# Kernel tuning notes

Measured on AMD Instinct MI355X. Metric: run time of the kernel, lower is better.

## Reference

```python
import jax, jax.numpy as jnp
import numpy as np

B, T, C = 2, 2048, 1024
E = 8            # num_experts
K = 2            # num_active (top-k)
H = 4 * C        # expert hidden dim


def setup_inputs() -> dict:
    key = jax.random.key(0)
    ks = jax.random.split(key, 8)
    s = 0.02
    return {
        "x": jax.random.normal(ks[0], (B, T, C), dtype=jnp.float32),
        "Wg": jax.random.normal(ks[1], (C, E), dtype=jnp.float32) * s,
        "bg": jnp.zeros((E,), dtype=jnp.float32),
        "W1": jax.random.normal(ks[2], (E, C, H), dtype=jnp.float32) * s,
        "b1": jnp.zeros((E, H), dtype=jnp.float32),
        "W2": jax.random.normal(ks[3], (E, H, C), dtype=jnp.float32) * s,
        "b2": jnp.zeros((E, C), dtype=jnp.float32),
    }


def reference(x, Wg, bg, W1, b1, W2, b2):
    Bs, Ts, Cs = x.shape
    x_flat = x.reshape(-1, Cs)                       # [N, C]
    gate_logits = x_flat @ Wg + bg                   # [N, E]
    gates = jax.nn.softmax(gate_logits, axis=-1)
    w, idx = jax.lax.top_k(gates, K)                 # [N, K]
    w = w / jnp.sum(w, axis=-1, keepdims=True)
    # combine[n, e] = sum_k w[n,k] * (idx[n,k] == e); zero for unrouted experts,
    # so weighting the dense per-expert output reproduces the masked scatter-add.
    combine = jnp.sum(jax.nn.one_hot(idx, E, dtype=x.dtype) * w[..., None], axis=1)  # [N, E]
    out = jnp.zeros_like(x_flat)
    for e in range(E):  # small fixed expert loop; GEMM-dominated
        h = jax.nn.gelu(x_flat @ W1[e] + b1[e], approximate=False)  # [N, H]
        y = h @ W2[e] + b2[e]                                       # [N, C]
        out = out + y * combine[:, e:e + 1]
    return out.reshape(Bs, Ts, Cs)
```

## Files before the change

kernel.cpp:

```cpp
#include <hip/hip_runtime.h>
#include <hip/hip_bf16.h>
#include <math.h>

#define NTOK  4096
#define CDIM  1024
#define HDIM  4096
#define NEXP  8
#define MAXROWS (NTOK * 2 + NEXP * 128)
#define MAXTILES 72

using short8 = __attribute__((ext_vector_type(8))) short;
using f32x4  = __attribute__((ext_vector_type(4))) float;
using us4    = __attribute__((ext_vector_type(4))) unsigned short;
using us8    = __attribute__((ext_vector_type(8))) unsigned short;

__device__ inline ushort f2bf(float f) {
    uint32_t u = __builtin_bit_cast(uint32_t, f);
    uint32_t r = (u + 0x7FFFu + ((u >> 16) & 1u)) >> 16;
    return (ushort)r;
}

__device__ __forceinline__ void gl_lds16(const void* g, void* l) {
    __builtin_amdgcn_global_load_lds(
        (const __attribute__((address_space(1))) void*)(void*)g,
        (__attribute__((address_space(3))) void*)l, 16, 0, 0);
}

__global__ __launch_bounds__(256)
void gate_kernel(const float* __restrict__ x, const float* __restrict__ Wg,
                 const float* __restrict__ bg, int* __restrict__ counts,
                 int4* __restrict__ tchoice, float2* __restrict__ tw) {
    int wave = threadIdx.x >> 6, lane = threadIdx.x & 63;
    int t = blockIdx.x * 4 + wave;
    const float* xr = x + (size_t)t * CDIM;

    float acc[NEXP];
#pragma unroll
    for (int e = 0; e < NEXP; e++) acc[e] = 0.f;

#pragma unroll
    for (int i = 0; i < CDIM / 64; i++) {
        int c = lane + 64 * i;
        float xv = xr[c];
        const float4* wr = (const float4*)(Wg + (size_t)c * NEXP);
        float4 w0 = wr[0], w1 = wr[1];
        acc[0] += xv * w0.x; acc[1] += xv * w0.y;
        acc[2] += xv * w0.z; acc[3] += xv * w0.w;
        acc[4] += xv * w1.x; acc[5] += xv * w1.y;
        acc[6] += xv * w1.z; acc[7] += xv * w1.w;
    }
#pragma unroll
    for (int e = 0; e < NEXP; e++) {
        float v = acc[e];
        for (int off = 32; off > 0; off >>= 1) v += __shfl_xor(v, off);
        acc[e] = v + bg[e];
    }
    if (lane == 0) {
        int i1 = 0; float m1 = acc[0];
#pragma unroll
        for (int e = 1; e < NEXP; e++) if (acc[e] > m1) { m1 = acc[e]; i1 = e; }
        int i2 = -1; float m2 = -1e30f;
#pragma unroll
        for (int e = 0; e < NEXP; e++) if (e != i1 && acc[e] > m2) { m2 = acc[e]; i2 = e; }
        float w0 = 1.f / (1.f + expf(m2 - m1));
        float w1 = 1.f - w0;
        int p0 = atomicAdd(&counts[i1], 1);
        int p1 = atomicAdd(&counts[i2], 1);
        tchoice[t] = make_int4(i1, p0, i2, p1);
        tw[t] = make_float2(w0, w1);
    }
}

__global__ void scan_kernel(const int* __restrict__ counts, int* __restrict__ bases,
                            int* __restrict__ tmeta) {
    if (threadIdx.x == 0) {
        int b = 0, nt = 0;
        for (int e = 0; e < NEXP; e++) {
            bases[e] = b;
            int tiles = (counts[e] + 127) >> 7;
            for (int m = 0; m < tiles; m++) tmeta[1 + nt++] = (e << 16) | m;
            b += tiles << 7;
        }
        tmeta[0] = nt;
    }
}

__global__ __launch_bounds__(256)
void pack_kernel(const float* __restrict__ x, const int4* __restrict__ tchoice,
                 const float2* __restrict__ tw, const int* __restrict__ bases,
                 ushort* __restrict__ xpack, float* __restrict__ wpack,
                 int* __restrict__ tokpack) {
    int t = blockIdx.x, tid = threadIdx.x;
    int4 ch = tchoice[t];
    float2 wv = tw[t];
    int d1 = bases[ch.x] + ch.y;
    int d2 = bases[ch.z] + ch.w;
    float4 v = ((const float4*)(x + (size_t)t * CDIM))[tid];
    us4 o;
    o[0] = f2bf(v.x); o[1] = f2bf(v.y); o[2] = f2bf(v.z); o[3] = f2bf(v.w);
    *(us4*)&xpack[(size_t)d1 * CDIM + tid * 4] = o;
    *(us4*)&xpack[(size_t)d2 * CDIM + tid * 4] = o;
    if (tid == 0) {
        wpack[d1] = wv.x; tokpack[d1] = t;
        wpack[d2] = wv.y; tokpack[d2] = t;
    }
}

__global__ __launch_bounds__(256)
void transpose_kernel(const float* __restrict__ in, ushort* __restrict__ out,
                      int R, int Cc) {
    __shared__ float tile[64 * 65];
    int e = blockIdx.z;
    const float* src = in + (size_t)e * R * Cc;
    ushort* dst = out + (size_t)e * Cc * R;
    int c0 = blockIdx.x * 64, r0 = blockIdx.y * 64;
    int tid = threadIdx.x, tx = tid & 15, ty = tid >> 4;
#pragma unroll
    for (int j = 0; j < 4; j++) {
        float4 v = *(const float4*)&src[(size_t)(r0 + ty + 16 * j) * Cc + c0 + tx * 4];
        int base = (ty + 16 * j) * 65 + tx * 4;
        tile[base + 0] = v.x; tile[base + 1] = v.y;
        tile[base + 2] = v.z; tile[base + 3] = v.w;
    }
    __syncthreads();
    int rb = tid & 7, ccb = tid >> 3;
#pragma unroll
    for (int p = 0; p < 2; p++) {
        int cc = ccb + 32 * p;
        us8 o;
#pragma unroll
        for (int i = 0; i < 8; i++) o[i] = f2bf(tile[(rb * 8 + i) * 65 + cc]);
        *(us8*)&dst[(size_t)(c0 + cc) * R + r0 + rb * 8] = o;
    }
}

template<int GELU, int ATOMIC>
__global__ __launch_bounds__(256)
void moe_gemm(const ushort* __restrict__ A, const ushort* __restrict__ Bt,
              const float* __restrict__ bias, const int* __restrict__ tmeta,
              const int* __restrict__ counts, const int* __restrict__ bases,
              ushort* __restrict__ outH, float* __restrict__ outA,
              const float* __restrict__ wpack, const int* __restrict__ tokpack,
              int K, int N) {
    int ti = blockIdx.y;
    if (ti >= tmeta[0]) return;
    int packed = tmeta[1 + ti];
    int e  = packed >> 16;
    int m0 = (packed & 0xffff) << 7;
    int n0 = blockIdx.x * 128;
    int kspan = K / gridDim.z;
    int k0 = blockIdx.z * kspan;
    int cnt = counts[e], base = bases[e];

    const ushort* Ae = A + (size_t)base * K;
    const ushort* Be = Bt + (size_t)e * N * K;

    __shared__ ushort As[128 * 32];
    __shared__ ushort Bs[128 * 32];

    int tid = threadIdx.x, lane = tid & 63, w = tid >> 6;
    int wm = (w >> 1) * 64, wn = (w & 1) * 64;
    int quad = lane >> 4, l16 = lane & 15;
    int srow = tid >> 2;
    int scol = (tid & 3) * 8;

    f32x4 acc[4][4] = {};

    for (int kt = k0; kt < k0 + kspan; kt += 32) {
#pragma unroll
        for (int s = 0; s < 2; s++) {
            int row = srow + s * 64;
            gl_lds16(Ae + (size_t)(m0 + row) * K + kt + scol, &As[(w * 16 + s * 64) * 32]);
            gl_lds16(Be + (size_t)(n0 + row) * K + kt + scol, &Bs[(w * 16 + s * 64) * 32]);
        }
        __syncthreads();

        short8 a[4], b[4];
#pragma unroll
        for (int mt = 0; mt < 4; mt++)
            a[mt] = *(short8*)&As[(wm + mt * 16 + l16) * 32 + quad * 8];
#pragma unroll
        for (int nt = 0; nt < 4; nt++)
            b[nt] = *(short8*)&Bs[(wn + nt * 16 + l16) * 32 + quad * 8];
#pragma unroll
        for (int mt = 0; mt < 4; mt++)
#pragma unroll
            for (int nt = 0; nt < 4; nt++)
                acc[mt][nt] = __builtin_amdgcn_mfma_f32_16x16x32_bf16(
                    a[mt], b[nt], acc[mt][nt], 0, 0, 0);
        __syncthreads();
    }

    const float* be = bias + (size_t)e * N;
#pragma unroll
    for (int mt = 0; mt < 4; mt++) {
#pragma unroll
        for (int r = 0; r < 4; r++) {
            int lrow = wm + mt * 16 + quad * 4 + r;
            if (m0 + lrow < cnt) {
                int prow = base + m0 + lrow;
                if (GELU) {
                    size_t ob = (size_t)prow * N;
#pragma unroll
                    for (int nt = 0; nt < 4; nt++) {
                        int col = n0 + wn + nt * 16 + l16;
                        float val = acc[mt][nt][r] + be[col];
                        val = 0.5f * val * (1.0f + erff(val * 0.70710678118654752f));
                        outH[ob + col] = f2bf(val);
                    }
                }
                if (ATOMIC) {
                    float wv = wpack[prow];
                    size_t ob = (size_t)tokpack[prow] * CDIM;
#pragma unroll
                    for (int nt = 0; nt < 4; nt++) {
                        int col = n0 + wn + nt * 16 + l16;
                        float val = acc[mt][nt][r];
                        if (blockIdx.z == 0) val += be[col];
                        atomicAdd(&outA[ob + col], val * wv);
                    }
                }
            }
        }
    }
}

extern "C" void kernel_launch(void* const* d_in, const int* in_sizes, int n_in,
                              void* d_out, int out_size, void* d_ws, size_t ws_size,
                              hipStream_t stream) {
    const float* x  = (const float*)d_in[0];
    const float* Wg = (const float*)d_in[1];
    const float* bg = (const float*)d_in[2];
    const float* W1 = (const float*)d_in[3];
    const float* b1 = (const float*)d_in[4];
    const float* W2 = (const float*)d_in[5];
    const float* b2 = (const float*)d_in[6];
    float* out = (float*)d_out;
    char* ws = (char*)d_ws;

    size_t off = 0;
    int*    counts  = (int*)(ws + off);    off += 256;
    int*    bases   = (int*)(ws + off);    off += 256;
    int*    tmeta   = (int*)(ws + off);    off += 512;
    int4*   tchoice = (int4*)(ws + off);   off += (size_t)NTOK * 16;
    float2* tw      = (float2*)(ws + off); off += (size_t)NTOK * 8;
    float*  wpack   = (float*)(ws + off);  off += (size_t)MAXROWS * 4;
    int*    tokpack = (int*)(ws + off);    off += (size_t)MAXROWS * 4;
    off = (off + 255) & ~(size_t)255;
    ushort* xpack   = (ushort*)(ws + off); off += (size_t)MAXROWS * CDIM * 2;
    ushort* WT      = (ushort*)(ws + off); off += (size_t)NEXP * CDIM * HDIM * 2;
    ushort* h       = (ushort*)(ws + off); off += (size_t)MAXROWS * HDIM * 2;

    hipMemsetAsync(counts, 0, 256, stream);
    hipMemsetAsync(out, 0, (size_t)NTOK * CDIM * 4, stream);

    gate_kernel<<<NTOK / 4, 256, 0, stream>>>(x, Wg, bg, counts, tchoice, tw);
    scan_kernel<<<1, 64, 0, stream>>>(counts, bases, tmeta);
    pack_kernel<<<NTOK, 256, 0, stream>>>(x, tchoice, tw, bases, xpack, wpack, tokpack);

    transpose_kernel<<<dim3(HDIM / 64, CDIM / 64, NEXP), 256, 0, stream>>>(
        W1, WT, CDIM, HDIM);

    moe_gemm<1, 0><<<dim3(HDIM / 128, MAXTILES, 1), 256, 0, stream>>>(
        xpack, WT, b1, tmeta, counts, bases, h, nullptr, nullptr, nullptr,
        CDIM, HDIM);

    transpose_kernel<<<dim3(CDIM / 64, HDIM / 64, NEXP), 256, 0, stream>>>(
        W2, WT, HDIM, CDIM);

    moe_gemm<0, 1><<<dim3(CDIM / 128, MAXTILES, 2), 256, 0, stream>>>(
        h, WT, b2, tmeta, counts, bases, nullptr, out, wpack, tokpack,
        HDIM, CDIM);
}
```

Before: 753.6 us.

## Replace token packing with gather-indexed GEMM loads and fuse bf16 cast into gating

Drops the separate pack kernel: the gate kernel now writes a per-expert token-slot list and converts x to bf16 once, and both GEMMs gather A rows indirectly through a per-tile row index table in shared memory. The hidden activations are stored per token slot instead of per packed row. The second GEMM no longer splits K across two z-slices, which halves its atomic traffic but leaves fewer blocks to fill the GPU. Gathered row loads can lose some locality compared with contiguous packed rows.

```diff
diff --git a/kernel.cpp b/kernel.cpp
--- a/kernel.cpp
+++ b/kernel.cpp
@@ -6,7 +6,7 @@
 #define CDIM  1024
 #define HDIM  4096
 #define NEXP  8
-#define MAXROWS (NTOK * 2 + NEXP * 128)
+#define NSLOT (NTOK * 2)
 #define MAXTILES 72
 
 using short8 = __attribute__((ext_vector_type(8))) short;
@@ -29,86 +29,72 @@
 __global__ __launch_bounds__(256)
 void gate_kernel(const float* __restrict__ x, const float* __restrict__ Wg,
                  const float* __restrict__ bg, int* __restrict__ counts,
-                 int4* __restrict__ tchoice, float2* __restrict__ tw) {
-    int wave = threadIdx.x >> 6, lane = threadIdx.x & 63;
-    int t = blockIdx.x * 4 + wave;
-    const float* xr = x + (size_t)t * CDIM;
-
-    float acc[NEXP];
-#pragma unroll
-    for (int e = 0; e < NEXP; e++) acc[e] = 0.f;
-
-#pragma unroll
-    for (int i = 0; i < CDIM / 64; i++) {
-        int c = lane + 64 * i;
-        float xv = xr[c];
-        const float4* wr = (const float4*)(Wg + (size_t)c * NEXP);
-        float4 w0 = wr[0], w1 = wr[1];
-        acc[0] += xv * w0.x; acc[1] += xv * w0.y;
-        acc[2] += xv * w0.z; acc[3] += xv * w0.w;
-        acc[4] += xv * w1.x; acc[5] += xv * w1.y;
-        acc[6] += xv * w1.z; acc[7] += xv * w1.w;
-    }
-#pragma unroll
-    for (int e = 0; e < NEXP; e++) {
-        float v = acc[e];
-        for (int off = 32; off > 0; off >>= 1) v += __shfl_xor(v, off);
-        acc[e] = v + bg[e];
-    }
-    if (lane == 0) {
-        int i1 = 0; float m1 = acc[0];
-#pragma unroll
-        for (int e = 1; e < NEXP; e++) if (acc[e] > m1) { m1 = acc[e]; i1 = e; }
-        int i2 = -1; float m2 = -1e30f;
-#pragma unroll
-        for (int e = 0; e < NEXP; e++) if (e != i1 && acc[e] > m2) { m2 = acc[e]; i2 = e; }
-        float w0 = 1.f / (1.f + expf(m2 - m1));
-        float w1 = 1.f - w0;
-        int p0 = atomicAdd(&counts[i1], 1);
-        int p1 = atomicAdd(&counts[i2], 1);
-        tchoice[t] = make_int4(i1, p0, i2, p1);
-        tw[t] = make_float2(w0, w1);
-    }
-}
-
-__global__ void scan_kernel(const int* __restrict__ counts, int* __restrict__ bases,
-                            int* __restrict__ tmeta) {
+                 int* __restrict__ tlist, float* __restrict__ wslot,
+                 ushort* __restrict__ xbf) {
+    __shared__ float wgs[NEXP * CDIM];
+    int tid = threadIdx.x;
+#pragma unroll
+    for (int i = 0; i < CDIM; i += 32) {
+        int c = i + (tid >> 3), e = tid & 7;
+        wgs[e * CDIM + c] = Wg[c * NEXP + e];
+    }
+    __syncthreads();
+
+    int wave = tid >> 6, lane = tid & 63;
+#pragma unroll
+    for (int j = 0; j < 4; j++) {
+        int t = blockIdx.x * 16 + wave * 4 + j;
+        const float* xr = x + (size_t)t * CDIM;
+        float acc[NEXP];
+#pragma unroll
+        for (int e = 0; e < NEXP; e++) acc[e] = 0.f;
+#pragma unroll
+        for (int i = 0; i < CDIM / 64; i++) {
+            int c = lane + 64 * i;
+            float xv = xr[c];
+            xbf[(size_t)t * CDIM + c] = f2bf(xv);
+#pragma unroll
+            for (int e = 0; e < NEXP; e++) acc[e] += xv * wgs[e * CDIM + c];
+        }
+#pragma unroll
+        for (int e = 0; e < NEXP; e++) {
+            float v = acc[e];
+            for (int off = 32; off > 0; off >>= 1) v += __shfl_xor(v, off);
+            acc[e] = v + bg[e];
+        }
+        if (lane == 0) {
+            int i1 = 0; float m1 = acc[0];
+#pragma unroll
+            for (int e = 1; e < NEXP; e++) if (acc[e] > m1) { m1 = acc[e]; i1 = e; }
+            int i2 = -1; float m2 = -1e30f;
+#pragma unroll
+            for (int e = 0; e < NEXP; e++) if (e != i1 && acc[e] > m2) { m2 = acc[e]; i2 = e; }
+            float w0 = 1.f / (1.f + expf(m2 - m1));
+            float w1 = 1.f - w0;
+            int p0 = atomicAdd(&counts[i1], 1);
+            tlist[i1 * NTOK + p0] = t * 2;
+            int p1 = atomicAdd(&counts[i2], 1);
+            tlist[i2 * NTOK + p1] = t * 2 + 1;
+            wslot[t * 2]     = w0;
+            wslot[t * 2 + 1] = w1;
+        }
+    }
+}
+
+__global__ void scan_kernel(const int* __restrict__ counts, int* __restrict__ tmeta) {
     if (threadIdx.x == 0) {
-        int b = 0, nt = 0;
+        int nt = 0;
         for (int e = 0; e < NEXP; e++) {
-            bases[e] = b;
             int tiles = (counts[e] + 127) >> 7;
             for (int m = 0; m < tiles; m++) tmeta[1 + nt++] = (e << 16) | m;
-            b += tiles << 7;
         }
         tmeta[0] = nt;
     }
 }
 
-__global__ __launch_bounds__(256)
-void pack_kernel(const float* __restrict__ x, const int4* __restrict__ tchoice,
-                 const float2* __restrict__ tw, const int* __restrict__ bases,
-                 ushort* __restrict__ xpack, float* __restrict__ wpack,
-                 int* __restrict__ tokpack) {
-    int t = blockIdx.x, tid = threadIdx.x;
-    int4 ch = tchoice[t];
-    float2 wv = tw[t];
-    int d1 = bases[ch.x] + ch.y;
-    int d2 = bases[ch.z] + ch.w;
-    float4 v = ((const float4*)(x + (size_t)t * CDIM))[tid];
-    us4 o;
-    o[0] = f2bf(v.x); o[1] = f2bf(v.y); o[2] = f2bf(v.z); o[3] = f2bf(v.w);
-    *(us4*)&xpack[(size_t)d1 * CDIM + tid * 4] = o;
-    *(us4*)&xpack[(size_t)d2 * CDIM + tid * 4] = o;
-    if (tid == 0) {
-        wpack[d1] = wv.x; tokpack[d1] = t;
-        wpack[d2] = wv.y; tokpack[d2] = t;
-    }
-}
-
-__global__ __launch_bounds__(256)
-void transpose_kernel(const float* __restrict__ in, ushort* __restrict__ out,
-                      int R, int Cc) {
+__device__ __forceinline__
+void transpose_body(const float* __restrict__ in, ushort* __restrict__ out,
+                    int R, int Cc) {
     __shared__ float tile[64 * 65];
     int e = blockIdx.z;
     const float* src = in + (size_t)e * R * Cc;
@@ -133,44 +119,57 @@
         *(us8*)&dst[(size_t)(c0 + cc) * R + r0 + rb * 8] = o;
     }
 }
-
-template<int GELU, int ATOMIC>
-__global__ __launch_bounds__(256)
-void moe_gemm(const ushort* __restrict__ A, const ushort* __restrict__ Bt,
-              const float* __restrict__ bias, const int* __restrict__ tmeta,
-              const int* __restrict__ counts, const int* __restrict__ bases,
-              ushort* __restrict__ outH, float* __restrict__ outA,
-              const float* __restrict__ wpack, const int* __restrict__ tokpack,
-              int K, int N) {
+__global__ __launch_bounds__(256)
+void tr_w1_kernel(const float* __restrict__ in, ushort* __restrict__ out) {
+    transpose_body(in, out, CDIM, HDIM);
+}
+__global__ __launch_bounds__(256)
+void tr_w2_kernel(const float* __restrict__ in, ushort* __restrict__ out) {
+    transpose_body(in, out, HDIM, CDIM);
+}
+
+template<int MODE>
+__device__ __forceinline__
+void gemm_core(const ushort* __restrict__ A, const ushort* __restrict__ Bt,
+               const float* __restrict__ bias, const int* __restrict__ tmeta,
+               const int* __restrict__ tlist, const int* __restrict__ counts,
+               ushort* __restrict__ outH, float* __restrict__ outA,
+               const float* __restrict__ wslot, int K, int N) {
     int ti = blockIdx.y;
     if (ti >= tmeta[0]) return;
     int packed = tmeta[1 + ti];
     int e  = packed >> 16;
     int m0 = (packed & 0xffff) << 7;
     int n0 = blockIdx.x * 128;
-    int kspan = K / gridDim.z;
-    int k0 = blockIdx.z * kspan;
-    int cnt = counts[e], base = bases[e];
-
-    const ushort* Ae = A + (size_t)base * K;
-    const ushort* Be = Bt + (size_t)e * N * K;
+    int cnt = counts[e];
 
     __shared__ ushort As[128 * 32];
     __shared__ ushort Bs[128 * 32];
-
-    int tid = threadIdx.x, lane = tid & 63, w = tid >> 6;
+    __shared__ int rowv[128];
+
+    int tid = threadIdx.x;
+    if (tid < 128) {
+        int r = m0 + tid;
+        rowv[tid] = tlist[e * NTOK + (r < cnt ? r : cnt - 1)];
+    }
+    __syncthreads();
+
+    const ushort* Be = Bt + (size_t)e * N * K;
+
+    f32x4 acc[4][4] = {};
+
+    int lane = tid & 63, w = tid >> 6;
     int wm = (w >> 1) * 64, wn = (w & 1) * 64;
     int quad = lane >> 4, l16 = lane & 15;
     int srow = tid >> 2;
     int scol = (tid & 3) * 8;
 
-    f32x4 acc[4][4] = {};
-
-    for (int kt = k0; kt < k0 + kspan; kt += 32) {
+    for (int kt = 0; kt < K; kt += 32) {
 #pragma unroll
         for (int s = 0; s < 2; s++) {
             int row = srow + s * 64;
-            gl_lds16(Ae + (size_t)(m0 + row) * K + kt + scol, &As[(w * 16 + s * 64) * 32]);
+            int arow = MODE == 0 ? (rowv[row] >> 1) : rowv[row];
+            gl_lds16(A + (size_t)arow * K + kt + scol, &As[(w * 16 + s * 64) * 32]);
             gl_lds16(Be + (size_t)(n0 + row) * K + kt + scol, &Bs[(w * 16 + s * 64) * 32]);
         }
         __syncthreads();
@@ -198,9 +197,9 @@
         for (int r = 0; r < 4; r++) {
             int lrow = wm + mt * 16 + quad * 4 + r;
             if (m0 + lrow < cnt) {
-                int prow = base + m0 + lrow;
-                if (GELU) {
-                    size_t ob = (size_t)prow * N;
+                int v = rowv[lrow];
+                if (MODE == 0) {
+                    size_t ob = (size_t)v * N;
 #pragma unroll
                     for (int nt = 0; nt < 4; nt++) {
                         int col = n0 + wn + nt * 16 + l16;
@@ -208,21 +207,35 @@
                         val = 0.5f * val * (1.0f + erff(val * 0.70710678118654752f));
                         outH[ob + col] = f2bf(val);
                     }
-                }
-                if (ATOMIC) {
-                    float wv = wpack[prow];
-                    size_t ob = (size_t)tokpack[prow] * CDIM;
+                } else {
+                    float wv = wslot[v];
+                    size_t ob = (size_t)(v >> 1) * CDIM;
 #pragma unroll
                     for (int nt = 0; nt < 4; nt++) {
                         int col = n0 + wn + nt * 16 + l16;
-                        float val = acc[mt][nt][r];
-                        if (blockIdx.z == 0) val += be[col];
-                        atomicAdd(&outA[ob + col], val * wv);
+                        atomicAdd(&outA[ob + col], (acc[mt][nt][r] + be[col]) * wv);
                     }
                 }
             }
         }
     }
+}
+
+__global__ __launch_bounds__(256)
+void gemm1_kernel(const ushort* __restrict__ A, const ushort* __restrict__ Bt,
+                  const float* __restrict__ bias, const int* __restrict__ tmeta,
+                  const int* __restrict__ tlist, const int* __restrict__ counts,
+                  ushort* __restrict__ outH) {
+    gemm_core<0>(A, Bt, bias, tmeta, tlist, counts, outH, nullptr, nullptr,
+                 CDIM, HDIM);
+}
+__global__ __launch_bounds__(256)
+void gemm2_kernel(const ushort* __restrict__ A, const ushort* __restrict__ Bt,
+                  const float* __restrict__ bias, const int* __restrict__ tmeta,
+                  const int* __restrict__ tlist, const int* __restrict__ counts,
+                  float* __restrict__ outA, const float* __restrict__ wslot) {
+    gemm_core<1>(A, Bt, bias, tmeta, tlist, counts, nullptr, outA, wslot,
+                 HDIM, CDIM);
 }
 
 extern "C" void kernel_launch(void* const* d_in, const int* in_sizes, int n_in,
@@ -239,36 +252,28 @@
     char* ws = (char*)d_ws;
 
     size_t off = 0;
-    int*    counts  = (int*)(ws + off);    off += 256;
-    int*    bases   = (int*)(ws + off);    off += 256;
-    int*    tmeta   = (int*)(ws + off);    off += 512;
-    int4*   tchoice = (int4*)(ws + off);   off += (size_t)NTOK * 16;
-    float2* tw      = (float2*)(ws + off); off += (size_t)NTOK * 8;
-    float*  wpack   = (float*)(ws + off);  off += (size_t)MAXROWS * 4;
-    int*    tokpack = (int*)(ws + off);    off += (size_t)MAXROWS * 4;
+    int*    counts = (int*)(ws + off);    off += 256;
+    int*    tmeta  = (int*)(ws + off);    off += 512;
+    int*    tlist  = (int*)(ws + off);    off += (size_t)NEXP * NTOK * 4;
+    float*  wslot  = (float*)(ws + off);  off += (size_t)NSLOT * 4;
     off = (off + 255) & ~(size_t)255;
-    ushort* xpack   = (ushort*)(ws + off); off += (size_t)MAXROWS * CDIM * 2;
-    ushort* WT      = (ushort*)(ws + off); off += (size_t)NEXP * CDIM * HDIM * 2;
-    ushort* h       = (ushort*)(ws + off); off += (size_t)MAXROWS * HDIM * 2;
+    ushort* xbf    = (ushort*)(ws + off); off += (size_t)NTOK * CDIM * 2;
+    ushort* WT     = (ushort*)(ws + off); off += (size_t)NEXP * CDIM * HDIM * 2;
+    ushort* h      = (ushort*)(ws + off); off += (size_t)NSLOT * HDIM * 2;
 
     hipMemsetAsync(counts, 0, 256, stream);
     hipMemsetAsync(out, 0, (size_t)NTOK * CDIM * 4, stream);
 
-    gate_kernel<<<NTOK / 4, 256, 0, stream>>>(x, Wg, bg, counts, tchoice, tw);
-    scan_kernel<<<1, 64, 0, stream>>>(counts, bases, tmeta);
-    pack_kernel<<<NTOK, 256, 0, stream>>>(x, tchoice, tw, bases, xpack, wpack, tokpack);
-
-    transpose_kernel<<<dim3(HDIM / 64, CDIM / 64, NEXP), 256, 0, stream>>>(
-        W1, WT, CDIM, HDIM);
-
-    moe_gemm<1, 0><<<dim3(HDIM / 128, MAXTILES, 1), 256, 0, stream>>>(
-        xpack, WT, b1, tmeta, counts, bases, h, nullptr, nullptr, nullptr,
-        CDIM, HDIM);
-
-    transpose_kernel<<<dim3(CDIM / 64, HDIM / 64, NEXP), 256, 0, stream>>>(
-        W2, WT, HDIM, CDIM);
-
-    moe_gemm<0, 1><<<dim3(CDIM / 128, MAXTILES, 2), 256, 0, stream>>>(
-        h, WT, b2, tmeta, counts, bases, nullptr, out, wpack, tokpack,
-        HDIM, CDIM);
-}
+    gate_kernel<<<NTOK / 16, 256, 0, stream>>>(x, Wg, bg, counts, tlist, wslot, xbf);
+    scan_kernel<<<1, 64, 0, stream>>>(counts, tmeta);
+
+    tr_w1_kernel<<<dim3(HDIM / 64, CDIM / 64, NEXP), 256, 0, stream>>>(W1, WT);
+
+    gemm1_kernel<<<dim3(HDIM / 128, MAXTILES, 1), 256, 0, stream>>>(
+        xbf, WT, b1, tmeta, tlist, counts, h);
+
+    tr_w2_kernel<<<dim3(CDIM / 64, HDIM / 64, NEXP), 256, 0, stream>>>(W2, WT);
+
+    gemm2_kernel<<<dim3(CDIM / 128, MAXTILES, 1), 256, 0, stream>>>(
+        h, WT, b2, tmeta, tlist, counts, out, wslot);
+}
```

After: 711.5 us. -5.6%, faster.
